# Kernel optimization log

Measured on AMD Instinct MI355X. Metric: run time of the kernel, lower is better.

## Reference

```python
import jax, jax.numpy as jnp
import numpy as np


def setup_inputs() -> dict:
    key = jax.random.key(0)
    kq, kk, kv, ks = jax.random.split(key, 4)
    B, Sq, H, Hkv, D, Dv, Smax = 4, 4, 32, 8, 128, 128, 8192
    Q = jax.random.normal(kq, (B, Sq, H, D), dtype=jnp.float32)
    K = jax.random.normal(kk, (B, Smax, Hkv, D), dtype=jnp.float32)
    V = jax.random.normal(kv, (B, Smax, Hkv, Dv), dtype=jnp.float32)
    # cache lengths well inside [Sq, Smax]
    cache_seqlens = jax.random.randint(ks, (B,), 4096, Smax + 1, dtype=jnp.int32)
    return {"Q": Q, "K": K, "V": V, "cache_seqlens": cache_seqlens}


def reference(Q, K, V, cache_seqlens):
    # Q: [B, Sq, H, D]; K: [B, Smax, Hkv, D]; V: [B, Smax, Hkv, Dv]
    B, Sq, H, D = Q.shape
    Smax, Hkv = K.shape[1], K.shape[2]
    g = H // Hkv  # GQA group size
    scale = 1.0 / (D ** 0.5)

    # Group query heads by their shared KV head to avoid repeating K/V.
    Qg = Q.reshape(B, Sq, Hkv, g, D)
    # scores: [B, Hkv, g, Sq, Smax]
    scores = jnp.einsum("bqhgd,bkhd->bhgqk", Qg, K) * scale

    # Causal-at-cache-end mask: position j valid iff j <= cache_seqlens[b] - Sq + m
    pos = jnp.arange(Smax)
    limit = cache_seqlens[:, None] - Sq + jnp.arange(Sq)[None, :]  # [B, Sq]
    mask = pos[None, None, :] <= limit[:, :, None]                 # [B, Sq, Smax]
    neg_inf = jnp.asarray(-jnp.inf, dtype=scores.dtype)
    scores = jnp.where(mask[:, None, None, :, :], scores, neg_inf)

    attn = jax.nn.softmax(scores, axis=-1)
    out = jnp.einsum("bhgqk,bkhd->bqhgd", attn, V)  # [B, Sq, Hkv, g, Dv]
    return out.reshape(B, Sq, H, V.shape[-1])
```

## Files before the change

kernel.cpp:

```cpp
#include <hip/hip_runtime.h>
#include <hip/hip_bf16.h>
#include <stdint.h>

#define B_    4
#define SQ    4
#define H_    32
#define HKV   8
#define G_    4
#define D_    128
#define SMAX  8192
#define ROWS  16
#define BH    (B_ * HKV)
#define SCALE 0.08838834764831845f
#define C2    0.12751743f
#define MAXSPLITS 32
#define KSTRB 2048
#define LDS_K 0
#define LDS_V 16384

typedef short bf16x8 __attribute__((ext_vector_type(8)));
typedef float f32x4  __attribute__((ext_vector_type(4)));
typedef unsigned int u32x2 __attribute__((ext_vector_type(2)));
typedef unsigned int u32x4 __attribute__((ext_vector_type(4)));

__device__ __forceinline__ void unpack8(const uint4& u, float* f) {
  f[0] = __uint_as_float(u.x << 16);
  f[1] = __uint_as_float(u.x & 0xffff0000u);
  f[2] = __uint_as_float(u.y << 16);
  f[3] = __uint_as_float(u.y & 0xffff0000u);
  f[4] = __uint_as_float(u.z << 16);
  f[5] = __uint_as_float(u.z & 0xffff0000u);
  f[6] = __uint_as_float(u.w << 16);
  f[7] = __uint_as_float(u.w & 0xffff0000u);
}

__device__ __forceinline__ uint32_t bf16bits(float x) {
  __hip_bfloat16 h = __float2bfloat16(x);
  uint16_t u; __builtin_memcpy(&u, &h, 2);
  return (uint32_t)u;
}

__device__ __forceinline__ void g2lds16(const void* g, void* l) {
  __builtin_amdgcn_global_load_lds(
      (const __attribute__((address_space(1))) void*)g,
      (__attribute__((address_space(3))) void*)l, 16, 0, 0);
}

__global__ __launch_bounds__(256)
void fa4_sniff(const uint32_t* __restrict__ Kw, int* __restrict__ flag) {
  __shared__ int s_cnt;
  const int t = threadIdx.x;
  if (t == 0) s_cnt = 0;
  __syncthreads();
  int local = 0;
#pragma unroll
  for (int i = 0; i < 4; ++i) {
    const uint32_t w = Kw[t * 4 + i];
    const uint32_t e = (w >> 7) & 0xFFu;
    local += (e >= 100u && e <= 150u) ? 1 : 0;
  }
  atomicAdd(&s_cnt, local);
  __syncthreads();
  if (t == 0) flag[0] = (s_cnt > 700) ? 1 : 0;
}

__device__ __forceinline__ void partial_body_f32(
    const void* __restrict__ Q, const void* __restrict__ K,
    const void* __restrict__ V, const int* __restrict__ lens,
    int splits, int chunk,
    float* __restrict__ Lout, float* __restrict__ acc_out) {
  constexpr int KB = 8;

  const int split = blockIdx.x;
  const int bh    = blockIdx.y;
  const int b     = bh >> 3;
  const int hkv   = bh & 7;
  const int t     = threadIdx.x;
  const int r     = t >> 4;
  const int c     = t & 15;
  const int m     = r >> 2;
  const int gq    = r & 3;
  const int h     = hkv * G_ + gq;

  int len = lens[b];
  if (len > SMAX) len = SMAX;
  if (len < 0)    len = 0;

  const int j0   = split * chunk;
  const int jend = min(j0 + chunk, len);
  const int lim  = len - SQ + m;
  const int vend = min(jend, lim + 1);

  const int sidx = (bh * splits + split) * ROWS + r;
  float* ap = acc_out + (size_t)sidx * D_ + c * 8;

  if (j0 >= vend) {
    if (c == 0) Lout[sidx] = 0.0f;
    const float4 z = make_float4(0.f, 0.f, 0.f, 0.f);
    *(float4*)(ap)     = z;
    *(float4*)(ap + 4) = z;
    return;
  }

  float qf[8];
  {
    const float4* p = (const float4*)((const float*)Q +
        (size_t)(((b * SQ + m) * H_ + h) * D_) + c * 8);
    const float4 a0 = p[0], a1 = p[1];
    qf[0]=a0.x; qf[1]=a0.y; qf[2]=a0.z; qf[3]=a0.w;
    qf[4]=a1.x; qf[5]=a1.y; qf[6]=a1.z; qf[7]=a1.w;
#pragma unroll
    for (int i = 0; i < 8; ++i) qf[i] *= SCALE;
  }

  const size_t kv0 = ((size_t)b * SMAX * HKV + hkv) * D_ + c * 8;
  const char*  kbase = (const char*)K + kv0 * 4;
  const char*  vbase = (const char*)V + kv0 * 4;
  const size_t kstrb = (size_t)HKV * D_ * 4;

  float l_run  = 0.0f;
  float acc[8] = {0.f,0.f,0.f,0.f,0.f,0.f,0.f,0.f};

  int j = j0;
  for (; j + KB <= vend; j += KB) {
    uint4 kraw[KB][2], vraw[KB][2];
#pragma unroll
    for (int kb = 0; kb < KB; ++kb) {
      const char* kp = kbase + (size_t)(j + kb) * kstrb;
      const char* vp = vbase + (size_t)(j + kb) * kstrb;
#pragma unroll
      for (int q = 0; q < 2; ++q) {
        kraw[kb][q] = ((const uint4*)kp)[q];
        vraw[kb][q] = ((const uint4*)vp)[q];
      }
    }
    __builtin_amdgcn_sched_barrier(0);
    float lsum = 0.0f;
#pragma unroll
    for (int kb = 0; kb < KB; ++kb) {
      const float* kk = (const float*)&kraw[kb][0];
      const float* vv = (const float*)&vraw[kb][0];
      float p = qf[0] * kk[0];
#pragma unroll
      for (int i = 1; i < 8; ++i) p = fmaf(qf[i], kk[i], p);
      p += __shfl_xor(p, 1, 16);
      p += __shfl_xor(p, 2, 16);
      p += __shfl_xor(p, 4, 16);
      p += __shfl_xor(p, 8, 16);
      const float pw = __expf(p);
      lsum += pw;
#pragma unroll
      for (int i = 0; i < 8; ++i) acc[i] = fmaf(pw, vv[i], acc[i]);
    }
    l_run += lsum;
  }

  if (j < vend) {
    const int jmaxv = vend - 1;
    uint4 kraw[KB][2], vraw[KB][2];
#pragma unroll
    for (int kb = 0; kb < KB; ++kb) {
      const int jj = min(j + kb, jmaxv);
      const char* kp = kbase + (size_t)jj * kstrb;
      const char* vp = vbase + (size_t)jj * kstrb;
#pragma unroll
      for (int q = 0; q < 2; ++q) {
        kraw[kb][q] = ((const uint4*)kp)[q];
        vraw[kb][q] = ((const uint4*)vp)[q];
      }
    }
    __builtin_amdgcn_sched_barrier(0);
    float lsum = 0.0f;
#pragma unroll
    for (int kb = 0; kb < KB; ++kb) {
      const float* kk = (const float*)&kraw[kb][0];
      const float* vv = (const float*)&vraw[kb][0];
      float p = qf[0] * kk[0];
#pragma unroll
      for (int i = 1; i < 8; ++i) p = fmaf(qf[i], kk[i], p);
      p += __shfl_xor(p, 1, 16);
      p += __shfl_xor(p, 2, 16);
      p += __shfl_xor(p, 4, 16);
      p += __shfl_xor(p, 8, 16);
      const float pw = (j + kb <= jmaxv) ? __expf(p) : 0.0f;
      lsum += pw;
#pragma unroll
      for (int i = 0; i < 8; ++i) acc[i] = fmaf(pw, vv[i], acc[i]);
    }
    l_run += lsum;
  }

  if (c == 0) Lout[sidx] = l_run;
  *(float4*)(ap)     = make_float4(acc[0], acc[1], acc[2], acc[3]);
  *(float4*)(ap + 4) = make_float4(acc[4], acc[5], acc[6], acc[7]);
}

__device__ __forceinline__ void mfma_body(
    const void* __restrict__ Q, const void* __restrict__ K,
    const void* __restrict__ V, const int* __restrict__ lens,
    int splits, int chunk,
    float* __restrict__ Lout, float* __restrict__ acc_out, char* smem) {
  const int split = blockIdx.x;
  const int bh    = blockIdx.y;
  const int b     = bh >> 3;
  const int hkv   = bh & 7;
  const int t     = threadIdx.x;
  const int w     = t >> 6;
  const int lane  = t & 63;
  const int lg    = lane >> 4;
  const int lc    = lane & 15;

  int len = lens[b];
  if (len > SMAX) len = SMAX;
  if (len < 0)    len = 0;

  const int j0    = split * chunk;
  const int jend  = min(j0 + chunk, len);
  const int sbase = (bh * splits + split) * ROWS;

  if (j0 >= jend) {
    const int row = t >> 4, c = t & 15;
    float* ap = acc_out + (size_t)(sbase + row) * D_ + c * 8;
    const float4 z = make_float4(0.f, 0.f, 0.f, 0.f);
    *(float4*)ap = z; *(float4*)(ap + 4) = z;
    if (t < 16) Lout[sbase + t] = 0.f;
    return;
  }

  const int rho = lc, qm = rho >> 2, gq = rho & 3;
  const char* Qb = (const char*)Q;
  const size_t qbyte =
      (((size_t)(b * SQ + qm) * H_ + hkv * G_ + gq) * D_ + (size_t)lg * 8) * 2;
  bf16x8 qf[4];
#pragma unroll
  for (int kc = 0; kc < 4; ++kc)
    qf[kc] = *(const bf16x8*)(Qb + qbyte + kc * 64);

  const int vmax = min(jend - 1, len - SQ + qm);

  const size_t kvbyte0 = ((size_t)b * SMAX * HKV + hkv) * D_ * 2;
  const char* Kb = (const char*)K + kvbyte0;
  const char* Vb = (const char*)V + kvbyte0;

  f32x4 acc[8];
#pragma unroll
  for (int i = 0; i < 8; ++i) acc[i] = (f32x4)0.f;
  float Lacc = 0.f;

  for (int tb = j0; tb < jend; tb += 64) {
#pragma unroll
    for (int q = 0; q < 4; ++q) {
      const int idx  = (w * 4 + q) * 64 + lane;
      const int key  = idx >> 4;
      const int slot = idx & 15;
      const int j    = min(tb + key, len - 1);
      g2lds16(Kb + (size_t)j * KSTRB + (size_t)((slot ^ (key & 15)) << 4),
              smem + LDS_K + (w * 4 + q) * 1024);
    }
#pragma unroll
    for (int q = 0; q < 4; ++q) {
      const int cidx  = (w * 4 + q) * 64 + lane;
      const int dvh   = cidx & 1;
      const int key16 = (cidx >> 1) & 15;
      const int t8    = (cidx >> 5) & 7;
      const int sub2  = cidx >> 8;
      const int j     = min(tb + sub2 * 16 + key16, len - 1);
      g2lds16(Vb + (size_t)j * KSTRB + (size_t)(t8 * 32 + dvh * 16),
              smem + LDS_V + (w * 4 + q) * 1024);
    }
    __syncthreads();

    f32x4 s = (f32x4)0.f;
    const char* krow = smem + LDS_K + (w * 16 + lc) * 256;
#pragma unroll
    for (int kc = 0; kc < 4; ++kc) {
      bf16x8 kf = *(const bf16x8*)(krow + (((kc * 4 + lg) ^ lc) << 4));
      s = __builtin_amdgcn_mfma_f32_16x16x32_bf16(kf, qf[kc], s, 0, 0, 0);
    }

    const int key0 = tb + w * 16 + lg * 4;
    float pw[4];
#pragma unroll
    for (int j4 = 0; j4 < 4; ++j4)
      pw[j4] = (key0 + j4 <= vmax) ? exp2f(s[j4] * C2) : 0.f;
    Lacc += (pw[0] + pw[1]) + (pw[2] + pw[3]);

    uint32_t hb[4], lb[4];
#pragma unroll
    for (int j4 = 0; j4 < 4; ++j4) {
      hb[j4] = bf16bits(pw[j4]);
      const float hf = __uint_as_float(hb[j4] << 16);
      lb[j4] = bf16bits(pw[j4] - hf);
    }
    u32x4 pa;
    pa.x = hb[0] | (hb[1] << 16);
    pa.y = hb[2] | (hb[3] << 16);
    pa.z = lb[0] | (lb[1] << 16);
    pa.w = lb[2] | (lb[3] << 16);
    const bf16x8 pfrag = __builtin_bit_cast(bf16x8, pa);

    typedef __attribute__((address_space(3))) const char* ldsp;
    u32x2 tr[8];
    ldsp vb3 = (ldsp)(smem + LDS_V + w * 4096 + lg * 128 + lc * 2);
    asm volatile("ds_read_b64_tr_b16 %0, %1 offset:0"    : "=v"(tr[0]) : "v"(vb3));
    asm volatile("ds_read_b64_tr_b16 %0, %1 offset:512"  : "=v"(tr[1]) : "v"(vb3));
    asm volatile("ds_read_b64_tr_b16 %0, %1 offset:1024" : "=v"(tr[2]) : "v"(vb3));
    asm volatile("ds_read_b64_tr_b16 %0, %1 offset:1536" : "=v"(tr[3]) : "v"(vb3));
    asm volatile("ds_read_b64_tr_b16 %0, %1 offset:2048" : "=v"(tr[4]) : "v"(vb3));
    asm volatile("ds_read_b64_tr_b16 %0, %1 offset:2560" : "=v"(tr[5]) : "v"(vb3));
    asm volatile("ds_read_b64_tr_b16 %0, %1 offset:3072" : "=v"(tr[6]) : "v"(vb3));
    asm volatile("ds_read_b64_tr_b16 %0, %1 offset:3584" : "=v"(tr[7]) : "v"(vb3));
    asm volatile("s_waitcnt lgkmcnt(0)" ::: "memory");
    __builtin_amdgcn_sched_barrier(0);

#pragma unroll
    for (int t8 = 0; t8 < 8; ++t8) {
      u32x4 vv;
      vv.x = tr[t8].x; vv.y = tr[t8].y; vv.z = tr[t8].x; vv.w = tr[t8].y;
      const bf16x8 vf = __builtin_bit_cast(bf16x8, vv);
      acc[t8] = __builtin_amdgcn_mfma_f32_16x16x32_bf16(pfrag, vf, acc[t8], 0, 0, 0);
    }
    __syncthreads();
  }

  float* accbuf = (float*)smem;
  float* Lb     = (float*)(smem + 32768);
#pragma unroll
  for (int t8 = 0; t8 < 8; ++t8)
#pragma unroll
    for (int j4 = 0; j4 < 4; ++j4)
      accbuf[w * 2048 + (lg * 4 + j4) * 128 + t8 * 16 + lc] = acc[t8][j4];
  float Ls = Lacc;
  Ls += __shfl_xor(Ls, 16);
  Ls += __shfl_xor(Ls, 32);
  if (lane < 16) Lb[w * 16 + lane] = Ls;
  __syncthreads();

  const int row = t >> 4, c = t & 15;
  float o[8] = {0.f,0.f,0.f,0.f,0.f,0.f,0.f,0.f};
#pragma unroll
  for (int ww = 0; ww < 4; ++ww) {
    const float4* p = (const float4*)(accbuf + ww * 2048 + row * 128 + c * 8);
    const float4 a0 = p[0], a1 = p[1];
    o[0]+=a0.x; o[1]+=a0.y; o[2]+=a0.z; o[3]+=a0.w;
    o[4]+=a1.x; o[5]+=a1.y; o[6]+=a1.z; o[7]+=a1.w;
  }
  float* ap = acc_out + (size_t)(sbase + row) * D_ + c * 8;
  *(float4*)ap       = make_float4(o[0], o[1], o[2], o[3]);
  *(float4*)(ap + 4) = make_float4(o[4], o[5], o[6], o[7]);
  if (t < 16) Lout[sbase + t] = Lb[t] + Lb[16 + t] + Lb[32 + t] + Lb[48 + t];
}

__global__ __launch_bounds__(256, 2)
void fa4_partial(const void* __restrict__ Q, const void* __restrict__ K,
                 const void* __restrict__ V, const int* __restrict__ lens,
                 const int* __restrict__ flag, int splits, int chunk,
                 float* __restrict__ Lout, float* __restrict__ acc_out) {
  __shared__ char smem[33792];
  if (flag[0] == 1)
    mfma_body(Q, K, V, lens, splits, chunk, Lout, acc_out, smem);
  else
    partial_body_f32(Q, K, V, lens, splits, chunk, Lout, acc_out);
}

__global__ __launch_bounds__(256)
void fa4_reduce(const float* __restrict__ Lin,
                const float* __restrict__ acc_in,
                const int* __restrict__ flag, int splits,
                void* __restrict__ out) {
  const int bh  = blockIdx.x;
  const int b   = bh >> 3;
  const int hkv = bh & 7;
  const int t   = threadIdx.x;
  const int r   = t >> 4;
  const int c   = t & 15;
  const int m   = r >> 2;
  const int gq  = r & 3;
  const int h   = hkv * G_ + gq;

  float L = 0.0f;
  float o[8] = {0.f,0.f,0.f,0.f,0.f,0.f,0.f,0.f};
#pragma unroll 4
  for (int s = 0; s < splits; ++s) {
    const size_t row = (size_t)(bh * splits + s) * ROWS + r;
    L += Lin[row];
    const float4* ap = (const float4*)(acc_in + row * D_ + c * 8);
    const float4 a0 = ap[0];
    const float4 a1 = ap[1];
    o[0] += a0.x; o[1] += a0.y; o[2] += a0.z; o[3] += a0.w;
    o[4] += a1.x; o[5] += a1.y; o[6] += a1.z; o[7] += a1.w;
  }
  const float inv = (L > 0.0f) ? (1.0f / L) : 0.0f;
  const size_t oo = ((size_t)(b * SQ + m) * H_ + h) * D_ + c * 8;
  if (flag[0] == 1) {
    unsigned short us[8];
#pragma unroll
    for (int i = 0; i < 8; ++i) {
      const __hip_bfloat16 hb2 = __float2bfloat16(o[i] * inv);
      __builtin_memcpy(&us[i], &hb2, 2);
    }
    uint4 pk;
    pk.x = (uint32_t)us[0] | ((uint32_t)us[1] << 16);
    pk.y = (uint32_t)us[2] | ((uint32_t)us[3] << 16);
    pk.z = (uint32_t)us[4] | ((uint32_t)us[5] << 16);
    pk.w = (uint32_t)us[6] | ((uint32_t)us[7] << 16);
    *(uint4*)((__hip_bfloat16*)out + oo) = pk;
  } else {
    float* op = (float*)out + oo;
    *(float4*)(op)     = make_float4(o[0]*inv, o[1]*inv, o[2]*inv, o[3]*inv);
    *(float4*)(op + 4) = make_float4(o[4]*inv, o[5]*inv, o[6]*inv, o[7]*inv);
  }
}

extern "C" void kernel_launch(void* const* d_in, const int* in_sizes, int n_in,
                              void* d_out, int out_size, void* d_ws, size_t ws_size,
                              hipStream_t stream) {
  const void* Q   = d_in[0];
  const void* K   = d_in[1];
  const void* V   = d_in[2];
  const int* lens = (const int*)d_in[3];

  const size_t per_split = (size_t)BH * ROWS * sizeof(float)
                         + (size_t)BH * ROWS * D_ * sizeof(float);
  int S = 1;
  if (ws_size > 256 + per_split)
    S = (int)((ws_size - 256) / per_split);
  if (S < 1) S = 1;
  if (S > MAXSPLITS) S = MAXSPLITS;
  const int chunk = (SMAX + S - 1) / S;

  int*   flag = (int*)d_ws;
  float* Lbuf = (float*)((char*)d_ws + 256);
  float* acc  = (float*)((char*)d_ws + 256 + (size_t)S * BH * ROWS * sizeof(float));

  fa4_sniff<<<1, 256, 0, stream>>>((const uint32_t*)K, flag);

  dim3 g1(S, BH);
  fa4_partial<<<g1, 256, 0, stream>>>(Q, K, V, lens, flag, S, chunk, Lbuf, acc);
  fa4_reduce<<<BH, 256, 0, stream>>>(Lbuf, acc, flag, S, d_out);
}
```

Measured before the change: 392.9 us.

## Process all KV heads per block so contiguous K/V rows are loaded once

```diff
diff --git a/kernel.cpp b/kernel.cpp
--- a/kernel.cpp
+++ b/kernel.cpp
@@ -13,26 +13,16 @@
 #define BH    (B_ * HKV)
 #define SCALE 0.08838834764831845f
 #define C2    0.12751743f
-#define MAXSPLITS 32
+#define MAXSPLITS 64
 #define KSTRB 2048
+#define TILE  16
 #define LDS_K 0
-#define LDS_V 16384
+#define LDS_V 32768
 
 typedef short bf16x8 __attribute__((ext_vector_type(8)));
 typedef float f32x4  __attribute__((ext_vector_type(4)));
 typedef unsigned int u32x2 __attribute__((ext_vector_type(2)));
 typedef unsigned int u32x4 __attribute__((ext_vector_type(4)));
-
-__device__ __forceinline__ void unpack8(const uint4& u, float* f) {
-  f[0] = __uint_as_float(u.x << 16);
-  f[1] = __uint_as_float(u.x & 0xffff0000u);
-  f[2] = __uint_as_float(u.y << 16);
-  f[3] = __uint_as_float(u.y & 0xffff0000u);
-  f[4] = __uint_as_float(u.z << 16);
-  f[5] = __uint_as_float(u.z & 0xffff0000u);
-  f[6] = __uint_as_float(u.w << 16);
-  f[7] = __uint_as_float(u.w & 0xffff0000u);
-}
 
 __device__ __forceinline__ uint32_t bf16bits(float x) {
   __hip_bfloat16 h = __float2bfloat16(x);
@@ -72,15 +62,12 @@
   constexpr int KB = 8;
 
   const int split = blockIdx.x;
-  const int bh    = blockIdx.y;
-  const int b     = bh >> 3;
-  const int hkv   = bh & 7;
+  const int b     = blockIdx.y;
   const int t     = threadIdx.x;
   const int r     = t >> 4;
   const int c     = t & 15;
   const int m     = r >> 2;
   const int gq    = r & 3;
-  const int h     = hkv * G_ + gq;
 
   int len = lens[b];
   if (len > SMAX) len = SMAX;
@@ -91,108 +78,84 @@
   const int lim  = len - SQ + m;
   const int vend = min(jend, lim + 1);
 
-  const int sidx = (bh * splits + split) * ROWS + r;
-  float* ap = acc_out + (size_t)sidx * D_ + c * 8;
-
-  if (j0 >= vend) {
-    if (c == 0) Lout[sidx] = 0.0f;
-    const float4 z = make_float4(0.f, 0.f, 0.f, 0.f);
-    *(float4*)(ap)     = z;
-    *(float4*)(ap + 4) = z;
-    return;
-  }
-
-  float qf[8];
+  float qf0[8];
   {
-    const float4* p = (const float4*)((const float*)Q +
-        (size_t)(((b * SQ + m) * H_ + h) * D_) + c * 8);
-    const float4 a0 = p[0], a1 = p[1];
-    qf[0]=a0.x; qf[1]=a0.y; qf[2]=a0.z; qf[3]=a0.w;
-    qf[4]=a1.x; qf[5]=a1.y; qf[6]=a1.z; qf[7]=a1.w;
-#pragma unroll
-    for (int i = 0; i < 8; ++i) qf[i] *= SCALE;
-  }
-
-  const size_t kv0 = ((size_t)b * SMAX * HKV + hkv) * D_ + c * 8;
-  const char*  kbase = (const char*)K + kv0 * 4;
-  const char*  vbase = (const char*)V + kv0 * 4;
-  const size_t kstrb = (size_t)HKV * D_ * 4;
-
-  float l_run  = 0.0f;
-  float acc[8] = {0.f,0.f,0.f,0.f,0.f,0.f,0.f,0.f};
-
-  int j = j0;
-  for (; j + KB <= vend; j += KB) {
-    uint4 kraw[KB][2], vraw[KB][2];
-#pragma unroll
-    for (int kb = 0; kb < KB; ++kb) {
-      const char* kp = kbase + (size_t)(j + kb) * kstrb;
-      const char* vp = vbase + (size_t)(j + kb) * kstrb;
-#pragma unroll
-      for (int q = 0; q < 2; ++q) {
-        kraw[kb][q] = ((const uint4*)kp)[q];
-        vraw[kb][q] = ((const uint4*)vp)[q];
-      }
-    }
-    __builtin_amdgcn_sched_barrier(0);
-    float lsum = 0.0f;
-#pragma unroll
-    for (int kb = 0; kb < KB; ++kb) {
-      const float* kk = (const float*)&kraw[kb][0];
-      const float* vv = (const float*)&vraw[kb][0];
-      float p = qf[0] * kk[0];
-#pragma unroll
-      for (int i = 1; i < 8; ++i) p = fmaf(qf[i], kk[i], p);
-      p += __shfl_xor(p, 1, 16);
-      p += __shfl_xor(p, 2, 16);
-      p += __shfl_xor(p, 4, 16);
-      p += __shfl_xor(p, 8, 16);
-      const float pw = __expf(p);
-      lsum += pw;
-#pragma unroll
-      for (int i = 0; i < 8; ++i) acc[i] = fmaf(pw, vv[i], acc[i]);
-    }
-    l_run += lsum;
-  }
-
-  if (j < vend) {
+    const int h = gq;
+    (void)h;
+  }
+
+  for (int hkv = 0; hkv < HKV; ++hkv) {
+    const int h    = hkv * G_ + gq;
+    const int sidx = ((b * HKV + hkv) * splits + split) * ROWS + r;
+    float* ap = acc_out + (size_t)sidx * D_ + c * 8;
+
+    if (j0 >= vend) {
+      if (c == 0) Lout[sidx] = 0.0f;
+      const float4 z = make_float4(0.f, 0.f, 0.f, 0.f);
+      *(float4*)(ap)     = z;
+      *(float4*)(ap + 4) = z;
+      continue;
+    }
+
+    float qf[8];
+    {
+      const float4* p = (const float4*)((const float*)Q +
+          (size_t)(((b * SQ + m) * H_ + h) * D_) + c * 8);
+      const float4 a0 = p[0], a1 = p[1];
+      qf[0]=a0.x; qf[1]=a0.y; qf[2]=a0.z; qf[3]=a0.w;
+      qf[4]=a1.x; qf[5]=a1.y; qf[6]=a1.z; qf[7]=a1.w;
+#pragma unroll
+      for (int i = 0; i < 8; ++i) qf[i] *= SCALE;
+    }
+    (void)qf0;
+
+    const size_t kv0 = ((size_t)b * SMAX * HKV + hkv) * D_ + c * 8;
+    const char*  kbase = (const char*)K + kv0 * 4;
+    const char*  vbase = (const char*)V + kv0 * 4;
+    const size_t kstrb = (size_t)HKV * D_ * 4;
+
+    float l_run  = 0.0f;
+    float acc[8] = {0.f,0.f,0.f,0.f,0.f,0.f,0.f,0.f};
     const int jmaxv = vend - 1;
-    uint4 kraw[KB][2], vraw[KB][2];
-#pragma unroll
-    for (int kb = 0; kb < KB; ++kb) {
-      const int jj = min(j + kb, jmaxv);
-      const char* kp = kbase + (size_t)jj * kstrb;
-      const char* vp = vbase + (size_t)jj * kstrb;
-#pragma unroll
-      for (int q = 0; q < 2; ++q) {
-        kraw[kb][q] = ((const uint4*)kp)[q];
-        vraw[kb][q] = ((const uint4*)vp)[q];
-      }
-    }
-    __builtin_amdgcn_sched_barrier(0);
-    float lsum = 0.0f;
-#pragma unroll
-    for (int kb = 0; kb < KB; ++kb) {
-      const float* kk = (const float*)&kraw[kb][0];
-      const float* vv = (const float*)&vraw[kb][0];
-      float p = qf[0] * kk[0];
-#pragma unroll
-      for (int i = 1; i < 8; ++i) p = fmaf(qf[i], kk[i], p);
-      p += __shfl_xor(p, 1, 16);
-      p += __shfl_xor(p, 2, 16);
-      p += __shfl_xor(p, 4, 16);
-      p += __shfl_xor(p, 8, 16);
-      const float pw = (j + kb <= jmaxv) ? __expf(p) : 0.0f;
-      lsum += pw;
-#pragma unroll
-      for (int i = 0; i < 8; ++i) acc[i] = fmaf(pw, vv[i], acc[i]);
-    }
-    l_run += lsum;
-  }
-
-  if (c == 0) Lout[sidx] = l_run;
-  *(float4*)(ap)     = make_float4(acc[0], acc[1], acc[2], acc[3]);
-  *(float4*)(ap + 4) = make_float4(acc[4], acc[5], acc[6], acc[7]);
+
+    for (int j = j0; j < vend; j += KB) {
+      uint4 kraw[KB][2], vraw[KB][2];
+#pragma unroll
+      for (int kb = 0; kb < KB; ++kb) {
+        const int jj = min(j + kb, jmaxv);
+        const char* kp = kbase + (size_t)jj * kstrb;
+        const char* vp = vbase + (size_t)jj * kstrb;
+#pragma unroll
+        for (int q = 0; q < 2; ++q) {
+          kraw[kb][q] = ((const uint4*)kp)[q];
+          vraw[kb][q] = ((const uint4*)vp)[q];
+        }
+      }
+      __builtin_amdgcn_sched_barrier(0);
+      float lsum = 0.0f;
+#pragma unroll
+      for (int kb = 0; kb < KB; ++kb) {
+        const float* kk = (const float*)&kraw[kb][0];
+        const float* vv = (const float*)&vraw[kb][0];
+        float p = qf[0] * kk[0];
+#pragma unroll
+        for (int i = 1; i < 8; ++i) p = fmaf(qf[i], kk[i], p);
+        p += __shfl_xor(p, 1, 16);
+        p += __shfl_xor(p, 2, 16);
+        p += __shfl_xor(p, 4, 16);
+        p += __shfl_xor(p, 8, 16);
+        const float pw = (j + kb <= jmaxv) ? __expf(p) : 0.0f;
+        lsum += pw;
+#pragma unroll
+        for (int i = 0; i < 8; ++i) acc[i] = fmaf(pw, vv[i], acc[i]);
+      }
+      l_run += lsum;
+    }
+
+    if (c == 0) Lout[sidx] = l_run;
+    *(float4*)(ap)     = make_float4(acc[0], acc[1], acc[2], acc[3]);
+    *(float4*)(ap + 4) = make_float4(acc[4], acc[5], acc[6], acc[7]);
+  }
 }
 
 __device__ __forceinline__ void mfma_body(
@@ -201,9 +164,7 @@
     int splits, int chunk,
     float* __restrict__ Lout, float* __restrict__ acc_out, char* smem) {
   const int split = blockIdx.x;
-  const int bh    = blockIdx.y;
-  const int b     = bh >> 3;
-  const int hkv   = bh & 7;
+  const int b     = blockIdx.y;
   const int t     = threadIdx.x;
   const int w     = t >> 6;
   const int lane  = t & 63;
@@ -214,141 +175,152 @@
   if (len > SMAX) len = SMAX;
   if (len < 0)    len = 0;
 
-  const int j0    = split * chunk;
-  const int jend  = min(j0 + chunk, len);
-  const int sbase = (bh * splits + split) * ROWS;
+  const int j0   = split * chunk;
+  const int jend = min(j0 + chunk, len);
 
   if (j0 >= jend) {
-    const int row = t >> 4, c = t & 15;
-    float* ap = acc_out + (size_t)(sbase + row) * D_ + c * 8;
+    const int rr = t >> 1, ch = t & 1;
+    const int hk = rr >> 4, rho = rr & 15;
+    const int sidx = ((b * HKV + hk) * splits + split) * ROWS + rho;
+    float* ap = acc_out + (size_t)sidx * D_ + ch * 64;
     const float4 z = make_float4(0.f, 0.f, 0.f, 0.f);
-    *(float4*)ap = z; *(float4*)(ap + 4) = z;
-    if (t < 16) Lout[sbase + t] = 0.f;
+#pragma unroll
+    for (int i = 0; i < 16; ++i) ((float4*)ap)[i] = z;
+    if (t < 128)
+      Lout[((b * HKV + (t >> 4)) * splits + split) * ROWS + (t & 15)] = 0.f;
     return;
   }
 
-  const int rho = lc, qm = rho >> 2, gq = rho & 3;
+  const int qm   = lc >> 2, gq = lc & 3;
+  const int vmax = min(jend, len - SQ + qm + 1) - 1;
+
   const char* Qb = (const char*)Q;
-  const size_t qbyte =
-      (((size_t)(b * SQ + qm) * H_ + hkv * G_ + gq) * D_ + (size_t)lg * 8) * 2;
-  bf16x8 qf[4];
-#pragma unroll
-  for (int kc = 0; kc < 4; ++kc)
-    qf[kc] = *(const bf16x8*)(Qb + qbyte + kc * 64);
-
-  const int vmax = min(jend - 1, len - SQ + qm);
-
-  const size_t kvbyte0 = ((size_t)b * SMAX * HKV + hkv) * D_ * 2;
-  const char* Kb = (const char*)K + kvbyte0;
-  const char* Vb = (const char*)V + kvbyte0;
-
-  f32x4 acc[8];
-#pragma unroll
-  for (int i = 0; i < 8; ++i) acc[i] = (f32x4)0.f;
-  float Lacc = 0.f;
-
-  for (int tb = j0; tb < jend; tb += 64) {
-#pragma unroll
-    for (int q = 0; q < 4; ++q) {
-      const int idx  = (w * 4 + q) * 64 + lane;
-      const int key  = idx >> 4;
-      const int slot = idx & 15;
+  bf16x8 qf[2][4];
+#pragma unroll
+  for (int ai = 0; ai < 2; ++ai) {
+    const int h = (2 * w + ai) * G_ + gq;
+    const size_t qbyte =
+        (((size_t)(b * SQ + qm) * H_ + h) * D_) * 2;
+#pragma unroll
+    for (int kc = 0; kc < 4; ++kc)
+      qf[ai][kc] = *(const bf16x8*)(Qb + qbyte + (size_t)(kc * 4 + lg) * 16);
+  }
+
+  const char* Kb = (const char*)K + (size_t)b * SMAX * KSTRB;
+  const char* Vb = (const char*)V + (size_t)b * SMAX * KSTRB;
+
+  f32x4 acc[2][8];
+#pragma unroll
+  for (int ai = 0; ai < 2; ++ai)
+#pragma unroll
+    for (int d = 0; d < 8; ++d) acc[ai][d] = (f32x4)0.f;
+  float La[2] = {0.f, 0.f};
+
+  for (int tb = j0; tb < jend; tb += TILE) {
+    uint4 va[4], vbr[4];
+#pragma unroll
+    for (int i = 0; i < 4; ++i) {
+      const int tau  = i * 256 + t;
+      const int slot = tau & 127;
+      const int pair = tau >> 7;
+      const int jA = min(tb + pair * 2,     len - 1);
+      const int jB = min(tb + pair * 2 + 1, len - 1);
+      va[i]  = *(const uint4*)(Vb + (size_t)jA * KSTRB + slot * 16);
+      vbr[i] = *(const uint4*)(Vb + (size_t)jB * KSTRB + slot * 16);
+    }
+#pragma unroll
+    for (int q = 0; q < 8; ++q) {
+      const int cidx = (w * 8 + q) * 64 + lane;
+      const int key  = cidx >> 7;
+      const int slot = cidx & 127;
       const int j    = min(tb + key, len - 1);
-      g2lds16(Kb + (size_t)j * KSTRB + (size_t)((slot ^ (key & 15)) << 4),
-              smem + LDS_K + (w * 4 + q) * 1024);
-    }
-#pragma unroll
-    for (int q = 0; q < 4; ++q) {
-      const int cidx  = (w * 4 + q) * 64 + lane;
-      const int dvh   = cidx & 1;
-      const int key16 = (cidx >> 1) & 15;
-      const int t8    = (cidx >> 5) & 7;
-      const int sub2  = cidx >> 8;
-      const int j     = min(tb + sub2 * 16 + key16, len - 1);
-      g2lds16(Vb + (size_t)j * KSTRB + (size_t)(t8 * 32 + dvh * 16),
-              smem + LDS_V + (w * 4 + q) * 1024);
+      g2lds16(Kb + (size_t)j * KSTRB + (size_t)((slot ^ (key & 7)) << 4),
+              smem + LDS_K + (w * 8 + q) * 1024);
+    }
+#pragma unroll
+    for (int i = 0; i < 4; ++i) {
+      const int tau  = i * 256 + t;
+      const int slot = tau & 127;
+      const int pair = tau >> 7;
+      const int hk   = slot >> 4;
+      const int dvt  = (slot >> 1) & 7;
+      const int d0   = (slot & 1) * 8;
+      const int swz  = (dvt << 3) ^ ((hk & 1) << 6);
+      const uint32_t* aw = (const uint32_t*)&va[i];
+      const uint32_t* bw = (const uint32_t*)&vbr[i];
+      char* vt = smem + LDS_V + hk * 4096 + dvt * 512;
+#pragma unroll
+      for (int e = 0; e < 8; ++e) {
+        const uint32_t ae = (e & 1) ? (aw[e >> 1] >> 16) : (aw[e >> 1] & 0xffffu);
+        const uint32_t be = (e & 1) ? (bw[e >> 1] >> 16) : (bw[e >> 1] & 0xffffu);
+        const int off = (((d0 + e) * 32 + pair * 4) ^ swz);
+        *(uint32_t*)(vt + off) = ae | (be << 16);
+      }
     }
     __syncthreads();
 
-    f32x4 s = (f32x4)0.f;
-    const char* krow = smem + LDS_K + (w * 16 + lc) * 256;
-#pragma unroll
-    for (int kc = 0; kc < 4; ++kc) {
-      bf16x8 kf = *(const bf16x8*)(krow + (((kc * 4 + lg) ^ lc) << 4));
-      s = __builtin_amdgcn_mfma_f32_16x16x32_bf16(kf, qf[kc], s, 0, 0, 0);
-    }
-
-    const int key0 = tb + w * 16 + lg * 4;
-    float pw[4];
-#pragma unroll
-    for (int j4 = 0; j4 < 4; ++j4)
-      pw[j4] = (key0 + j4 <= vmax) ? exp2f(s[j4] * C2) : 0.f;
-    Lacc += (pw[0] + pw[1]) + (pw[2] + pw[3]);
-
-    uint32_t hb[4], lb[4];
-#pragma unroll
-    for (int j4 = 0; j4 < 4; ++j4) {
-      hb[j4] = bf16bits(pw[j4]);
-      const float hf = __uint_as_float(hb[j4] << 16);
-      lb[j4] = bf16bits(pw[j4] - hf);
-    }
-    u32x4 pa;
-    pa.x = hb[0] | (hb[1] << 16);
-    pa.y = hb[2] | (hb[3] << 16);
-    pa.z = lb[0] | (lb[1] << 16);
-    pa.w = lb[2] | (lb[3] << 16);
-    const bf16x8 pfrag = __builtin_bit_cast(bf16x8, pa);
-
-    typedef __attribute__((address_space(3))) const char* ldsp;
-    u32x2 tr[8];
-    ldsp vb3 = (ldsp)(smem + LDS_V + w * 4096 + lg * 128 + lc * 2);
-    asm volatile("ds_read_b64_tr_b16 %0, %1 offset:0"    : "=v"(tr[0]) : "v"(vb3));
-    asm volatile("ds_read_b64_tr_b16 %0, %1 offset:512"  : "=v"(tr[1]) : "v"(vb3));
-    asm volatile("ds_read_b64_tr_b16 %0, %1 offset:1024" : "=v"(tr[2]) : "v"(vb3));
-    asm volatile("ds_read_b64_tr_b16 %0, %1 offset:1536" : "=v"(tr[3]) : "v"(vb3));
-    asm volatile("ds_read_b64_tr_b16 %0, %1 offset:2048" : "=v"(tr[4]) : "v"(vb3));
-    asm volatile("ds_read_b64_tr_b16 %0, %1 offset:2560" : "=v"(tr[5]) : "v"(vb3));
-    asm volatile("ds_read_b64_tr_b16 %0, %1 offset:3072" : "=v"(tr[6]) : "v"(vb3));
-    asm volatile("ds_read_b64_tr_b16 %0, %1 offset:3584" : "=v"(tr[7]) : "v"(vb3));
-    asm volatile("s_waitcnt lgkmcnt(0)" ::: "memory");
-    __builtin_amdgcn_sched_barrier(0);
-
-#pragma unroll
-    for (int t8 = 0; t8 < 8; ++t8) {
-      u32x4 vv;
-      vv.x = tr[t8].x; vv.y = tr[t8].y; vv.z = tr[t8].x; vv.w = tr[t8].y;
-      const bf16x8 vf = __builtin_bit_cast(bf16x8, vv);
-      acc[t8] = __builtin_amdgcn_mfma_f32_16x16x32_bf16(pfrag, vf, acc[t8], 0, 0, 0);
+    const int key0 = tb + lg * 4;
+#pragma unroll
+    for (int ai = 0; ai < 2; ++ai) {
+      const int a = 2 * w + ai;
+      f32x4 s = (f32x4)0.f;
+      const char* krow = smem + LDS_K + lc * KSTRB;
+#pragma unroll
+      for (int kc = 0; kc < 4; ++kc) {
+        const int slot = a * 16 + kc * 4 + lg;
+        const bf16x8 kf =
+            *(const bf16x8*)(krow + ((slot ^ (lc & 7)) << 4));
+        s = __builtin_amdgcn_mfma_f32_16x16x32_bf16(kf, qf[ai][kc], s, 0, 0, 0);
+      }
+      float pw[4];
+#pragma unroll
+      for (int j4 = 0; j4 < 4; ++j4)
+        pw[j4] = (key0 + j4 <= vmax) ? exp2f(s[j4] * C2) : 0.f;
+      La[ai] += (pw[0] + pw[1]) + (pw[2] + pw[3]);
+
+      uint32_t hb[4], lb[4];
+#pragma unroll
+      for (int j4 = 0; j4 < 4; ++j4) {
+        hb[j4] = bf16bits(pw[j4]);
+        const float hf = __uint_as_float(hb[j4] << 16);
+        lb[j4] = bf16bits(pw[j4] - hf);
+      }
+      u32x4 pa;
+      pa.x = hb[0] | (hb[1] << 16);
+      pa.y = hb[2] | (hb[3] << 16);
+      pa.z = lb[0] | (lb[1] << 16);
+      pa.w = lb[2] | (lb[3] << 16);
+      const bf16x8 pfrag = __builtin_bit_cast(bf16x8, pa);
+
+      const char* vt = smem + LDS_V + a * 4096;
+#pragma unroll
+      for (int dvt = 0; dvt < 8; ++dvt) {
+        const int off = ((lc * 32 + lg * 8) ^ ((dvt << 3) ^ ((a & 1) << 6)));
+        const u32x2 rb = *(const u32x2*)(vt + dvt * 512 + off);
+        u32x4 vv; vv.x = rb.x; vv.y = rb.y; vv.z = rb.x; vv.w = rb.y;
+        const bf16x8 vf = __builtin_bit_cast(bf16x8, vv);
+        acc[ai][dvt] =
+            __builtin_amdgcn_mfma_f32_16x16x32_bf16(pfrag, vf, acc[ai][dvt], 0, 0, 0);
+      }
     }
     __syncthreads();
   }
 
-  float* accbuf = (float*)smem;
-  float* Lb     = (float*)(smem + 32768);
-#pragma unroll
-  for (int t8 = 0; t8 < 8; ++t8)
-#pragma unroll
-    for (int j4 = 0; j4 < 4; ++j4)
-      accbuf[w * 2048 + (lg * 4 + j4) * 128 + t8 * 16 + lc] = acc[t8][j4];
-  float Ls = Lacc;
-  Ls += __shfl_xor(Ls, 16);
-  Ls += __shfl_xor(Ls, 32);
-  if (lane < 16) Lb[w * 16 + lane] = Ls;
-  __syncthreads();
-
-  const int row = t >> 4, c = t & 15;
-  float o[8] = {0.f,0.f,0.f,0.f,0.f,0.f,0.f,0.f};
-#pragma unroll
-  for (int ww = 0; ww < 4; ++ww) {
-    const float4* p = (const float4*)(accbuf + ww * 2048 + row * 128 + c * 8);
-    const float4 a0 = p[0], a1 = p[1];
-    o[0]+=a0.x; o[1]+=a0.y; o[2]+=a0.z; o[3]+=a0.w;
-    o[4]+=a1.x; o[5]+=a1.y; o[6]+=a1.z; o[7]+=a1.w;
-  }
-  float* ap = acc_out + (size_t)(sbase + row) * D_ + c * 8;
-  *(float4*)ap       = make_float4(o[0], o[1], o[2], o[3]);
-  *(float4*)(ap + 4) = make_float4(o[4], o[5], o[6], o[7]);
-  if (t < 16) Lout[sbase + t] = Lb[t] + Lb[16 + t] + Lb[32 + t] + Lb[48 + t];
+#pragma unroll
+  for (int ai = 0; ai < 2; ++ai) {
+    const int a = 2 * w + ai;
+    const int sbase = ((b * HKV + a) * splits + split) * ROWS;
+    float Ls = La[ai];
+    Ls += __shfl_xor(Ls, 16);
+    Ls += __shfl_xor(Ls, 32);
+    if (lane < 16) Lout[sbase + lane] = Ls;
+#pragma unroll
+    for (int dvt = 0; dvt < 8; ++dvt)
+#pragma unroll
+      for (int j4 = 0; j4 < 4; ++j4)
+        acc_out[(size_t)(sbase + lg * 4 + j4) * D_ + dvt * 16 + lc] =
+            acc[ai][dvt][j4];
+  }
 }
 
 __global__ __launch_bounds__(256, 2)
@@ -356,7 +328,7 @@
                  const void* __restrict__ V, const int* __restrict__ lens,
                  const int* __restrict__ flag, int splits, int chunk,
                  float* __restrict__ Lout, float* __restrict__ acc_out) {
-  __shared__ char smem[33792];
+  __shared__ char smem[65536];
   if (flag[0] == 1)
     mfma_body(Q, K, V, lens, splits, chunk, Lout, acc_out, smem);
   else
@@ -427,7 +399,7 @@
     S = (int)((ws_size - 256) / per_split);
   if (S < 1) S = 1;
   if (S > MAXSPLITS) S = MAXSPLITS;
-  const int chunk = (SMAX + S - 1) / S;
+  const int chunk = (((SMAX + S - 1) / S) + TILE - 1) & ~(TILE - 1);
 
   int*   flag = (int*)d_ws;
   float* Lbuf = (float*)((char*)d_ws + 256);
@@ -435,7 +407,7 @@
 
   fa4_sniff<<<1, 256, 0, stream>>>((const uint32_t*)K, flag);
 
-  dim3 g1(S, BH);
+  dim3 g1(S, B_);
   fa4_partial<<<g1, 256, 0, stream>>>(Q, K, V, lens, flag, S, chunk, Lbuf, acc);
   fa4_reduce<<<BH, 256, 0, stream>>>(Lbuf, acc, flag, S, d_out);
 }
```

Result: slower. 402.4 us (+2.4%).
